# Optimization experiments

Hardware: AMD Instinct MI355X
Metric: run time of the kernel (lower is better)

Reference implementation:

```python
import jax, jax.numpy as jnp
import numpy as np

B, T, D, HD, HN, O = 32, 512, 512, 64, 16, 512
EPS = 1e-5


def setup_inputs() -> dict:
    key = jax.random.key(0)
    ks = jax.random.split(key, 12)
    s = lambda fan_in: 1.0 / np.sqrt(fan_in)
    inp = {
        "inputs": jax.random.normal(ks[0], (B, T, D), dtype=jnp.float32),
        "Wq": jax.random.uniform(ks[1], (HN, D, HD), jnp.float32, -s(D), s(D)),
        "bq": jnp.zeros((HN, HD), jnp.float32),
        "Wk": jax.random.uniform(ks[2], (HN, D, HD), jnp.float32, -s(D), s(D)),
        "bk": jnp.zeros((HN, HD), jnp.float32),
        "Wv": jax.random.uniform(ks[3], (HN, D, HD), jnp.float32, -s(D), s(D)),
        "bv": jnp.zeros((HN, HD), jnp.float32),
        "Wr": jax.random.uniform(ks[4], (D, O), jnp.float32, -s(D), s(D)),
        "br": jnp.zeros((O,), jnp.float32),
        "Wo": jax.random.uniform(ks[5], (HN * HD, O), jnp.float32, -s(HN * HD), s(HN * HD)),
        "bo": jnp.zeros((O,), jnp.float32),
        "ln1_w": jnp.ones((O,), jnp.float32),
        "ln1_b": jnp.zeros((O,), jnp.float32),
        "Wfc": jax.random.uniform(ks[6], (O, O), jnp.float32, -s(O), s(O)),
        "bfc": jnp.zeros((O,), jnp.float32),
        "ln2_w": jnp.ones((O,), jnp.float32),
        "ln2_b": jnp.zeros((O,), jnp.float32),
    }
    return inp


def _layernorm(x, w, b):
    mu = jnp.mean(x, axis=-1, keepdims=True)
    var = jnp.mean(jnp.square(x - mu), axis=-1, keepdims=True)
    return (x - mu) * jax.lax.rsqrt(var + EPS) * w + b


def reference(inputs, Wq, bq, Wk, bk, Wv, bv, Wr, br, Wo, bo,
              ln1_w, ln1_b, Wfc, bfc, ln2_w, ln2_b):
    # causal mask: multiply-then-subtract as in the original
    score_mask = jnp.tril(jnp.ones((T, T), jnp.float32))        # [T,T]
    padding_mask = (score_mask == 0).astype(jnp.float32) * 1e9  # [T,T]

    residual = inputs @ Wr + br                                  # [B,T,O]

    # batched per-head projections with nonstandard activations
    q = jax.nn.relu(jnp.einsum('btd,hdf->bhtf', inputs, Wq) + bq[None, :, None, :])
    k = jax.nn.relu(jnp.einsum('btd,hdf->bhtf', inputs, Wk) + bk[None, :, None, :])
    v = jnp.tanh(jnp.einsum('btd,hdf->bhtf', inputs, Wv) + bv[None, :, None, :])

    scores = jnp.einsum('bhtf,bhsf->bhts', q, k) / jnp.sqrt(jnp.float32(HD))
    scores = scores * score_mask - padding_mask                  # [B,H,T,T]
    weights = jax.nn.softmax(scores, axis=-1)
    heads = jnp.einsum('bhts,bhsf->bhtf', weights, v)            # [B,H,T,HD]

    # concat heads (head order preserved) + tanh output projection
    concat = heads.transpose(0, 2, 1, 3).reshape(B, T, HN * HD)
    out = jnp.tanh(concat @ Wo + bo)                             # [B,T,O]

    out = _layernorm(out + residual, ln1_w, ln1_b)
    fc = jax.nn.relu(out @ Wfc + bfc)
    out = _layernorm(fc + out, ln2_w, ln2_b)
    return out
```

## Files before the change

### kernel.cpp

```cpp
#include <hip/hip_runtime.h>
#include <hip/hip_bf16.h>

#define B_  32
#define T_  512
#define D_  512
#define HD_ 64
#define HN_ 16
#define O_  512
#define M_  (B_ * T_)
#define NQ_ (HN_ * HD_)

typedef __bf16 bf16;
typedef __attribute__((ext_vector_type(8))) __bf16 bf16x8;
typedef __attribute__((ext_vector_type(4))) __bf16 bf16x4;
typedef __attribute__((ext_vector_type(4))) float f32x4;

static __device__ __forceinline__ f32x4 mfma16(bf16x8 a, bf16x8 b, f32x4 c) {
    return __builtin_amdgcn_mfma_f32_16x16x32_bf16(a, b, c, 0, 0, 0);
}

static __device__ __forceinline__ void load_lds_16B(const bf16* g, bf16* l) {
    __builtin_amdgcn_global_load_lds(
        (const __attribute__((address_space(1))) unsigned int*)(unsigned long long)g,
        (__attribute__((address_space(3))) unsigned int*)(unsigned long long)l,
        16, 0, 0);
}

static __device__ __forceinline__ float fast_tanh(float x) {
    return 1.f - 2.f / (__expf(2.f * x) + 1.f);
}

static __device__ __forceinline__ int2 swz_block() {
    const int nx = gridDim.x;
    const int nwg = nx * gridDim.y;
    int l = blockIdx.y * nx + blockIdx.x;
    l = (l & 7) * (nwg >> 3) + (l >> 3);
    return make_int2(l % nx, l / nx);
}

__global__ __launch_bounds__(256) void prep_all_kernel(
    const float* __restrict__ inputs,
    const float* __restrict__ Wq, const float* __restrict__ Wk,
    const float* __restrict__ Wv, const float* __restrict__ Wr,
    const float* __restrict__ Wo, const float* __restrict__ Wfc,
    const float* __restrict__ bq, const float* __restrict__ bk,
    const float* __restrict__ bv, const float* __restrict__ br,
    bf16* __restrict__ xin, bf16* __restrict__ wall,
    bf16* __restrict__ wrt, bf16* __restrict__ wot, bf16* __restrict__ wfct,
    float* __restrict__ ball)
{
    __shared__ bf16 tl[64][72];
    const int tid = threadIdx.x;
    int id = blockIdx.x;

    if (id < 4096) {
        const size_t i = ((size_t)id * 256 + tid) * 8;
        f32x4 x0 = *(const f32x4*)(inputs + i);
        f32x4 x1 = *(const f32x4*)(inputs + i + 4);
        bf16x8 v;
        v[0] = (bf16)x0[0]; v[1] = (bf16)x0[1]; v[2] = (bf16)x0[2]; v[3] = (bf16)x0[3];
        v[4] = (bf16)x1[0]; v[5] = (bf16)x1[1]; v[6] = (bf16)x1[2]; v[7] = (bf16)x1[3];
        *(bf16x8*)(xin + i) = v;
        return;
    }
    if (id < 4480) {
        id -= 4096;
        const int kt = id & 7; id >>= 3;
        const int h = id & 15; id >>= 4;
        const float* src = (id == 0) ? Wq : (id == 1) ? Wk : Wv;
        bf16* dst = wall + (size_t)id * (1024 * 512);
        const int k0 = kt * 64;
#pragma unroll
        for (int i = 0; i < 4; i++) {
            const int e = i * 256 + tid;
            const int kk = e >> 4, f4 = (e & 15) * 4;
            const f32x4 v = *(const f32x4*)(src + ((size_t)h * 512 + k0 + kk) * 64 + f4);
#pragma unroll
            for (int j = 0; j < 4; j++) tl[f4 + j][kk] = (bf16)v[j];
        }
        __syncthreads();
#pragma unroll
        for (int i = 0; i < 2; i++) {
            const int e = i * 256 + tid;
            const int f = e >> 3, kc = (e & 7) * 8;
            *(bf16x8*)(dst + ((size_t)h * 64 + f) * 512 + k0 + kc) = *(const bf16x8*)&tl[f][kc];
        }
        return;
    }
    if (id < 4736) {
        id -= 4480;
        const float* src; bf16* dst; int K;
        if (id < 64)       { src = Wr;  dst = wrt;  K = 512;  }
        else if (id < 192) { src = Wo;  dst = wot;  K = 1024; id -= 64; }
        else               { src = Wfc; dst = wfct; K = 512;  id -= 192; }
        const int kt = id >> 3, nt = id & 7;
        const int k0 = kt * 64, n0 = nt * 64;
#pragma unroll
        for (int i = 0; i < 4; i++) {
            const int e = i * 256 + tid;
            const int kk = e >> 4, n4 = (e & 15) * 4;
            const f32x4 v = *(const f32x4*)(src + (size_t)(k0 + kk) * 512 + n0 + n4);
#pragma unroll
            for (int j = 0; j < 4; j++) tl[n4 + j][kk] = (bf16)v[j];
        }
        __syncthreads();
#pragma unroll
        for (int i = 0; i < 2; i++) {
            const int e = i * 256 + tid;
            const int nn = e >> 3, kc = (e & 7) * 8;
            *(bf16x8*)(dst + (size_t)(n0 + nn) * K + k0 + kc) = *(const bf16x8*)&tl[nn][kc];
        }
        return;
    }
    const int i = (id - 4736) * 256 + tid;
    float v = (i < 1024) ? bq[i]
            : (i < 2048) ? bk[i - 1024]
            : (i < 3072) ? bv[i - 2048] : br[i - 3072];
    ball[i] = v;
}

__global__ __launch_bounds__(512, 2) void gemm_qkvr256_kernel(
    const bf16* __restrict__ A, const bf16* __restrict__ Wall,
    const float* __restrict__ ball,
    bf16* __restrict__ qc, bf16* __restrict__ kb, bf16* __restrict__ vt,
    bf16* __restrict__ resb)
{
    __shared__ bf16 SL[65536];
    const int tid = threadIdx.x;
    const int lane = tid & 63;
    const int w = tid >> 6;
    const int wm = w >> 2, wn = w & 3;
    const int lr = lane & 15, lg = lane >> 4;
    const int K = 512;

    const int2 bc = swz_block();
    const int m0 = bc.y * 256, n0 = bc.x * 256;

    const int p = tid & 7;
    const int rr = tid >> 3;
    const int g = p ^ (rr & 7);
    const int arow0 = rr, arow1 = 128 + rr;
    const int brow0 = ((rr >> 5) << 6) | (rr & 31);
    const int brow1 = 128 + brow0;

    auto STAGE_H = [&](int t, int h) {
        const int slot = t & 1;
        const int k0 = t << 6;
        if ((h & 1) == 0) {
            bf16* Bb = SL + 32768 + slot * 16384;
            const int off = (h == 2) ? 32 : 0;
            const int r0_ = brow0 + off, r1_ = brow1 + off;
            load_lds_16B(Wall + (size_t)(n0 + r0_) * K + k0 + g * 8, Bb + r0_ * 64 + p * 8);
            load_lds_16B(Wall + (size_t)(n0 + r1_) * K + k0 + g * 8, Bb + r1_ * 64 + p * 8);
        } else {
            bf16* Ab = SL + slot * 16384;
            const int off = (h == 3) ? 64 : 0;
            const int r0_ = arow0 + off, r1_ = arow1 + off;
            load_lds_16B(A + (size_t)(m0 + r0_) * K + k0 + g * 8, Ab + r0_ * 64 + p * 8);
            load_lds_16B(A + (size_t)(m0 + r1_) * K + k0 + g * 8, Ab + r1_ * 64 + p * 8);
        }
    };

    const int x = lr & 7;
    auto LDA = [&](int t, int mi, int kc) -> bf16x8 {
        const int row = wm * 128 + mi * 16 + lr;
        const bf16* Ab = SL + (t & 1) * 16384;
        return *(const bf16x8*)&Ab[row * 64 + ((((kc << 2) | lg) ^ x) << 3)];
    };
    auto LDB = [&](int t, int nj, int kc) -> bf16x8 {
        const int row = wn * 64 + nj * 16 + lr;
        const bf16* Bb = SL + 32768 + (t & 1) * 16384;
        return *(const bf16x8*)&Bb[row * 64 + ((((kc << 2) | lg) ^ x) << 3)];
    };

    f32x4 acc[8][4];
    const f32x4 zero4 = {0.f, 0.f, 0.f, 0.f};
#pragma unroll
    for (int i = 0; i < 8; i++)
#pragma unroll
        for (int j = 0; j < 4; j++) acc[i][j] = zero4;

    bf16x8 b01[4], b23[4], af[8];

    STAGE_H(0, 0); STAGE_H(0, 1); STAGE_H(0, 2); STAGE_H(0, 3);

    for (int t = 0; t < 7; t++) {
        asm volatile("s_waitcnt vmcnt(4)\n\ts_barrier" ::: "memory");
#pragma unroll
        for (int nj = 0; nj < 2; nj++)
#pragma unroll
            for (int kc = 0; kc < 2; kc++) b01[nj * 2 + kc] = LDB(t, nj, kc);
#pragma unroll
        for (int mi = 0; mi < 4; mi++)
#pragma unroll
            for (int kc = 0; kc < 2; kc++) af[mi * 2 + kc] = LDA(t, mi, kc);
        STAGE_H(t + 1, 0);
        __builtin_amdgcn_s_setprio(1);
#pragma unroll
        for (int mi = 0; mi < 4; mi++)
#pragma unroll
            for (int nj = 0; nj < 2; nj++)
#pragma unroll
                for (int kc = 0; kc < 2; kc++)
                    acc[mi][nj] = mfma16(af[mi * 2 + kc], b01[nj * 2 + kc], acc[mi][nj]);
        __builtin_amdgcn_s_setprio(0);
        asm volatile("s_waitcnt vmcnt(4)\n\ts_barrier" ::: "memory");
#pragma unroll
        for (int nj = 0; nj < 2; nj++)
#pragma unroll
            for (int kc = 0; kc < 2; kc++) b23[nj * 2 + kc] = LDB(t, nj + 2, kc);
        STAGE_H(t + 1, 1);
        __builtin_amdgcn_s_setprio(1);
#pragma unroll
        for (int mi = 0; mi < 4; mi++)
#pragma unroll
            for (int nj = 0; nj < 2; nj++)
#pragma unroll
                for (int kc = 0; kc < 2; kc++)
                    acc[mi][nj + 2] = mfma16(af[mi * 2 + kc], b23[nj * 2 + kc], acc[mi][nj + 2]);
        __builtin_amdgcn_s_setprio(0);
        asm volatile("s_waitcnt vmcnt(4)\n\ts_barrier" ::: "memory");
#pragma unroll
        for (int mi = 0; mi < 4; mi++)
#pragma unroll
            for (int kc = 0; kc < 2; kc++) af[mi * 2 + kc] = LDA(t, mi + 4, kc);
        STAGE_H(t + 1, 2);
        __builtin_amdgcn_s_setprio(1);
#pragma unroll
        for (int mi = 0; mi < 4; mi++)
#pragma unroll
            for (int nj = 0; nj < 2; nj++)
#pragma unroll
                for (int kc = 0; kc < 2; kc++)
                    acc[mi + 4][nj] = mfma16(af[mi * 2 + kc], b01[nj * 2 + kc], acc[mi + 4][nj]);
        __builtin_amdgcn_s_setprio(0);
        STAGE_H(t + 1, 3);
        __builtin_amdgcn_s_setprio(1);
#pragma unroll
        for (int mi = 0; mi < 4; mi++)
#pragma unroll
            for (int nj = 0; nj < 2; nj++)
#pragma unroll
                for (int kc = 0; kc < 2; kc++)
                    acc[mi + 4][nj + 2] = mfma16(af[mi * 2 + kc], b23[nj * 2 + kc], acc[mi + 4][nj + 2]);
        __builtin_amdgcn_s_setprio(0);
    }

    {
        const int t = 7;
        asm volatile("s_waitcnt vmcnt(4)\n\ts_barrier" ::: "memory");
#pragma unroll
        for (int nj = 0; nj < 2; nj++)
#pragma unroll
            for (int kc = 0; kc < 2; kc++) b01[nj * 2 + kc] = LDB(t, nj, kc);
#pragma unroll
        for (int mi = 0; mi < 4; mi++)
#pragma unroll
            for (int kc = 0; kc < 2; kc++) af[mi * 2 + kc] = LDA(t, mi, kc);
        __builtin_amdgcn_s_setprio(1);
#pragma unroll
        for (int mi = 0; mi < 4; mi++)
#pragma unroll
            for (int nj = 0; nj < 2; nj++)
#pragma unroll
                for (int kc = 0; kc < 2; kc++)
                    acc[mi][nj] = mfma16(af[mi * 2 + kc], b01[nj * 2 + kc], acc[mi][nj]);
        __builtin_amdgcn_s_setprio(0);
        asm volatile("s_waitcnt vmcnt(2)\n\ts_barrier" ::: "memory");
#pragma unroll
        for (int nj = 0; nj < 2; nj++)
#pragma unroll
            for (int kc = 0; kc < 2; kc++) b23[nj * 2 + kc] = LDB(t, nj + 2, kc);
        __builtin_amdgcn_s_setprio(1);
#pragma unroll
        for (int mi = 0; mi < 4; mi++)
#pragma unroll
            for (int nj = 0; nj < 2; nj++)
#pragma unroll
                for (int kc = 0; kc < 2; kc++)
                    acc[mi][nj + 2] = mfma16(af[mi * 2 + kc], b23[nj * 2 + kc], acc[mi][nj + 2]);
        __builtin_amdgcn_s_setprio(0);
        asm volatile("s_waitcnt vmcnt(0)\n\ts_barrier" ::: "memory");
#pragma unroll
        for (int mi = 0; mi < 4; mi++)
#pragma unroll
            for (int kc = 0; kc < 2; kc++) af[mi * 2 + kc] = LDA(t, mi + 4, kc);
        __builtin_amdgcn_s_setprio(1);
#pragma unroll
        for (int mi = 0; mi < 4; mi++)
#pragma unroll
            for (int nj = 0; nj < 2; nj++)
#pragma unroll
                for (int kc = 0; kc < 2; kc++)
                    acc[mi + 4][nj] = mfma16(af[mi * 2 + kc], b01[nj * 2 + kc], acc[mi + 4][nj]);
#pragma unroll
        for (int mi = 0; mi < 4; mi++)
#pragma unroll
            for (int nj = 0; nj < 2; nj++)
#pragma unroll
                for (int kc = 0; kc < 2; kc++)
                    acc[mi + 4][nj + 2] = mfma16(af[mi * 2 + kc], b23[nj * 2 + kc], acc[mi + 4][nj + 2]);
        __builtin_amdgcn_s_setprio(0);
    }
    __syncthreads();

    const int region = n0 >> 10;
    if (region == 2) {
#pragma unroll
        for (int mi = 0; mi < 8; mi++) {
#pragma unroll
            for (int nj = 0; nj < 4; nj++) {
                const int n = n0 + wn * 64 + nj * 16 + lr;
                const float bn = ball[n];
                const int m = m0 + wm * 128 + mi * 16 + lg * 4;
                const int bb = m >> 9, tt = m & 511;
                const int nn = n - 2048, hh = nn >> 6, f = nn & 63;
                bf16x4 st;
#pragma unroll
                for (int r = 0; r < 4; r++) st[r] = (bf16)fast_tanh(acc[mi][nj][r] + bn);
                *(bf16x4*)(vt + (((size_t)(bb * 16 + hh) * 64 + f) << 9) + tt) = st;
            }
        }
    } else {
        bf16* dst; int pitch, nb; float scale = 1.f; bool rl = false;
        if (region == 0)      { dst = qc;   pitch = 1024; nb = n0;        scale = 0.125f; rl = true; }
        else if (region == 1) { dst = kb;   pitch = 1024; nb = n0 - 1024; rl = true; }
        else                  { dst = resb; pitch = 512;  nb = n0 - 3072; }
        float bn[4];
#pragma unroll
        for (int nj = 0; nj < 4; nj++) bn[nj] = ball[n0 + wn * 64 + nj * 16 + lr];
#pragma unroll
        for (int half = 0; half < 2; half++) {
            if (wm == half) {
#pragma unroll
                for (int mi = 0; mi < 8; mi++) {
#pragma unroll
                    for (int nj = 0; nj < 4; nj++) {
                        const int col = wn * 64 + nj * 16 + lr;
#pragma unroll
                        for (int r = 0; r < 4; r++) {
                            float v = acc[mi][nj][r] + bn[nj];
                            if (rl) v = fmaxf(v, 0.f);
                            SL[(mi * 16 + lg * 4 + r) * 264 + col] = (bf16)(v * scale);
                        }
                    }
                }
            }
            __syncthreads();
#pragma unroll
            for (int i = 0; i < 4; i++) {
                const int rr2 = i * 32 + (tid >> 4);
                const int cc = (tid & 15) * 16;
                bf16x8 v0 = *(const bf16x8*)&SL[rr2 * 264 + cc];
                bf16x8 v1 = *(const bf16x8*)&SL[rr2 * 264 + cc + 8];
                bf16* pdst = dst + (size_t)(m0 + half * 128 + rr2) * pitch + nb + cc;
                *(bf16x8*)pdst = v0;
                *(bf16x8*)(pdst + 8) = v1;
            }
            __syncthreads();
        }
    }
}

__device__ __forceinline__ void gemm_mainloop_p4(
    const bf16* __restrict__ A, const bf16* __restrict__ Wt,
    const int K, const int m0, const int n0, const int tid,
    bf16* SL, f32x4 (&acc)[4][4])
{
    const int lane = tid & 63;
    const int w = tid >> 6;
    const int wr = w >> 1, wc = w & 1;
    const int lr = lane & 15, lg = lane >> 4;
    const int nt = K >> 5;

    const int r0 = tid >> 2, s0 = tid & 3;
    const int g0 = s0 ^ ((r0 >> 1) & 3);
    const int r1 = r0 + 64;
    const int g1 = s0 ^ ((r1 >> 1) & 3);
    const bf16* aS0 = A + (size_t)(m0 + r0) * K + g0 * 8;
    const bf16* aS1 = A + (size_t)(m0 + r1) * K + g1 * 8;
    const bf16* bS0 = Wt + (size_t)(n0 + r0) * K + g0 * 8;
    const bf16* bS1 = Wt + (size_t)(n0 + r1) * K + g1 * 8;

    auto STAGE = [&](int t) {
        bf16* Ab = SL + (t & 3) * 4096;
        bf16* Bb = SL + 16384 + (t & 3) * 4096;
        const int k0 = t << 5;
        load_lds_16B(aS0 + k0, Ab + tid * 8);
        load_lds_16B(aS1 + k0, Ab + (tid + 256) * 8);
        load_lds_16B(bS0 + k0, Bb + tid * 8);
        load_lds_16B(bS1 + k0, Bb + (tid + 256) * 8);
    };

    STAGE(0); STAGE(1);
    asm volatile("s_waitcnt vmcnt(4)" ::: "memory");
    __builtin_amdgcn_s_barrier();

    for (int t = 0; t < nt; t++) {
        if (t + 2 < nt) {
            STAGE(t + 2);
            asm volatile("s_waitcnt vmcnt(4)" ::: "memory");
        } else {
            asm volatile("s_waitcnt vmcnt(0)" ::: "memory");
        }
        __builtin_amdgcn_s_barrier();

        const bf16* Ab = SL + (t & 3) * 4096;
        const bf16* Bb = SL + 16384 + (t & 3) * 4096;
        bf16x8 a[4], b[4];
#pragma unroll
        for (int mi = 0; mi < 4; mi++) {
            const int row = wr * 64 + mi * 16 + lr;
            a[mi] = *(const bf16x8*)&Ab[row * 32 + ((lg ^ ((row >> 1) & 3)) << 3)];
        }
#pragma unroll
        for (int nj = 0; nj < 4; nj++) {
            const int row = wc * 64 + nj * 16 + lr;
            b[nj] = *(const bf16x8*)&Bb[row * 32 + ((lg ^ ((row >> 1) & 3)) << 3)];
        }
        __builtin_amdgcn_s_setprio(1);
#pragma unroll
        for (int mi = 0; mi < 4; mi++)
#pragma unroll
            for (int nj = 0; nj < 4; nj++)
                acc[mi][nj] = mfma16(a[mi], b[nj], acc[mi][nj]);
        __builtin_amdgcn_s_setprio(0);
    }
    __builtin_amdgcn_s_barrier();
}

template <int ACT>
__global__ __launch_bounds__(256) void gemm_std_kernel(
    const bf16* __restrict__ A, const bf16* __restrict__ Wt,
    const float* __restrict__ bias, bf16* __restrict__ C, const int K)
{
    __shared__ bf16 SL[32768];
    const int tid = threadIdx.x;
    const int2 bc = swz_block();
    const int m0 = bc.y * 128, n0 = bc.x * 128;
    f32x4 acc[4][4];
    const f32x4 zero4 = {0.f, 0.f, 0.f, 0.f};
#pragma unroll
    for (int i = 0; i < 4; i++)
#pragma unroll
        for (int j = 0; j < 4; j++) acc[i][j] = zero4;

    gemm_mainloop_p4(A, Wt, K, m0, n0, tid, SL, acc);

    const int lane = tid & 63, w = tid >> 6;
    const int wr = w >> 1, wc = w & 1, lr = lane & 15, lg = lane >> 4;
#pragma unroll
    for (int mi = 0; mi < 4; mi++) {
#pragma unroll
        for (int nj = 0; nj < 4; nj++) {
            const float bn = bias[n0 + wc * 64 + nj * 16 + lr];
            const int rbase = wr * 64 + mi * 16 + lg * 4;
            const int cidx = wc * 64 + nj * 16 + lr;
#pragma unroll
            for (int r = 0; r < 4; r++) {
                float v = acc[mi][nj][r] + bn;
                if constexpr (ACT == 1) v = fmaxf(v, 0.f);
                else if constexpr (ACT == 2) v = fast_tanh(v);
                SL[(rbase + r) * 136 + cidx] = (bf16)v;
            }
        }
    }
    __syncthreads();
#pragma unroll
    for (int pass = 0; pass < 4; pass++) {
        const int rr = pass * 32 + (tid >> 3);
        const int cc = (tid & 7) * 16;
        bf16x8 v0 = *(const bf16x8*)&SL[rr * 136 + cc];
        bf16x8 v1 = *(const bf16x8*)&SL[rr * 136 + cc + 8];
        *(bf16x8*)(C + (size_t)(m0 + rr) * 512 + n0 + cc) = v0;
        *(bf16x8*)(C + (size_t)(m0 + rr) * 512 + n0 + cc + 8) = v1;
    }
}

static __device__ __forceinline__ int sigma_k(int t) {
    return (t & 32) | ((t & 4) << 2) | ((t & 24) >> 1) | (t & 3);
}

__global__ __launch_bounds__(256) void mfma_attn_kernel(
    const bf16* __restrict__ Kb, const bf16* __restrict__ Vt, bf16* __restrict__ QC)
{
    __shared__ bf16 Ks[2][64][72];
    __shared__ bf16 Vts[2][64][72];

    int l = blockIdx.x;
    l = (l & 7) * 256 + (l >> 3);
    const int qb = l & 3;
    const int h = (l >> 2) & 15;
    const int b = l >> 6;
    const int tid = threadIdx.x;
    const int lane = tid & 63;
    const int w = tid >> 6;
    const int lr = lane & 15, lg = lane >> 4;

    const int qrow0 = qb * 128 + w * 32;
    const size_t qbase = ((size_t)b * T_ + qrow0) * NQ_ + h * 64;
    const int bh = b * HN_ + h;

    bf16x8 qf[2][2];
#pragma unroll
    for (int mi = 0; mi < 2; mi++)
#pragma unroll
        for (int kc = 0; kc < 2; kc++)
            qf[mi][kc] = *(const bf16x8*)(QC + qbase + (size_t)(mi * 16 + lr) * NQ_ + kc * 32 + lg * 8);

    const f32x4 zero4 = {0.f, 0.f, 0.f, 0.f};
    f32x4 o[2][4];
    float m_st[2] = {-1e30f, -1e30f}, l_st[2] = {0.f, 0.f};
#pragma unroll
    for (int mi = 0; mi < 2; mi++)
#pragma unroll
        for (int dj = 0; dj < 4; dj++) o[mi][dj] = zero4;

    const int nsb = 2 * qb + 2;

    bf16x8 kreg[2], vreg[2];
    auto LOADR = [&](int sb) {
#pragma unroll
        for (int i = 0; i < 2; i++) {
            const int ci = i * 256 + tid, row = ci >> 3, cc = ci & 7;
            kreg[i] = *(const bf16x8*)(Kb + ((size_t)b * T_ + sb * 64 + row) * NQ_ + h * 64 + cc * 8);
            vreg[i] = *(const bf16x8*)(Vt + ((size_t)bh * 64 + row) * T_ + sb * 64 + cc * 8);
        }
    };
    auto WRITE = [&](int buf) {
#pragma unroll
        for (int i = 0; i < 2; i++) {
            const int ci = i * 256 + tid, row = ci >> 3, cc = ci & 7;
            *(bf16x8*)&Ks[buf][sigma_k(row)][cc * 8] = kreg[i];
            *(bf16x8*)&Vts[buf][row][cc * 8] = vreg[i];
        }
    };

    LOADR(0); WRITE(0); __syncthreads();
    int cur = 0;

    for (int sb = 0; sb < nsb; sb++) {
        const bool pf = (sb + 1 < nsb);
        if (pf) LOADR(sb + 1);

        if (sb * 64 <= qrow0 + 31) {
            f32x4 sc[2][4];
#pragma unroll
            for (int mi = 0; mi < 2; mi++)
#pragma unroll
                for (int nj = 0; nj < 4; nj++) sc[mi][nj] = zero4;
            __builtin_amdgcn_s_setprio(1);
#pragma unroll
            for (int kc = 0; kc < 2; kc++) {
                bf16x8 kf[4];
#pragma unroll
                for (int nj = 0; nj < 4; nj++)
                    kf[nj] = *(const bf16x8*)&Ks[cur][nj * 16 + lr][kc * 32 + lg * 8];
#pragma unroll
                for (int mi = 0; mi < 2; mi++)
#pragma unroll
                    for (int nj = 0; nj < 4; nj++)
                        sc[mi][nj] = mfma16(kf[nj], qf[mi][kc], sc[mi][nj]);
            }
            __builtin_amdgcn_s_setprio(0);
            const bool needmask = (sb * 64 + 63 > qrow0);
            float tm[2];
#pragma unroll
            for (int mi = 0; mi < 2; mi++) {
                const int qg = qrow0 + mi * 16 + lr;
                float mx = -1e30f;
#pragma unroll
                for (int nj = 0; nj < 4; nj++) {
                    const int kvb = sb * 64 + ((nj >> 1) << 5) + ((nj & 1) << 2) + lg * 8;
#pragma unroll
                    for (int r = 0; r < 4; r++) {
                        float s = sc[mi][nj][r];
                        if (needmask && (kvb + r > qg)) s = -1e30f;
                        sc[mi][nj][r] = s;
                        mx = fmaxf(mx, s);
                    }
                }
                mx = fmaxf(mx, __shfl_xor(mx, 16));
                mx = fmaxf(mx, __shfl_xor(mx, 32));
                tm[mi] = mx;
            }
            const bool defer = (tm[0] <= m_st[0] + 8.f) && (tm[1] <= m_st[1] + 8.f);
            if (!__all(defer)) {
#pragma unroll
                for (int mi = 0; mi < 2; mi++) {
                    const float mn = fmaxf(m_st[mi], tm[mi]);
                    const float sf = __expf(m_st[mi] - mn);
                    m_st[mi] = mn;
                    l_st[mi] *= sf;
#pragma unroll
                    for (int dj = 0; dj < 4; dj++)
#pragma unroll
                        for (int r = 0; r < 4; r++) o[mi][dj][r] *= sf;
                }
            }
            bf16x4 pk[2][4];
#pragma unroll
            for (int mi = 0; mi < 2; mi++) {
                float ts = 0.f;
#pragma unroll
                for (int nj = 0; nj < 4; nj++)
#pragma unroll
                    for (int r = 0; r < 4; r++) {
                        const float p2 = __expf(sc[mi][nj][r] - m_st[mi]);
                        ts += p2;
                        pk[mi][nj][r] = (bf16)p2;
                    }
                ts += __shfl_xor(ts, 16);
                ts += __shfl_xor(ts, 32);
                l_st[mi] += ts;
            }
            __builtin_amdgcn_s_setprio(1);
#pragma unroll
            for (int kc = 0; kc < 2; kc++) {
                bf16x8 vf[4], pf2[2];
#pragma unroll
                for (int mi = 0; mi < 2; mi++) {
                    bf16x8 t;
#pragma unroll
                    for (int r = 0; r < 4; r++) { t[r] = pk[mi][2 * kc][r]; t[r + 4] = pk[mi][2 * kc + 1][r]; }
                    pf2[mi] = t;
                }
#pragma unroll
                for (int dj = 0; dj < 4; dj++)
                    vf[dj] = *(const bf16x8*)&Vts[cur][dj * 16 + lr][kc * 32 + lg * 8];
#pragma unroll
                for (int mi = 0; mi < 2; mi++)
#pragma unroll
                    for (int dj = 0; dj < 4; dj++)
                        o[mi][dj] = mfma16(vf[dj], pf2[mi], o[mi][dj]);
            }
            __builtin_amdgcn_s_setprio(0);
        }

        if (pf) WRITE(cur ^ 1);
        __syncthreads();
        cur ^= 1;
    }

#pragma unroll
    for (int mi = 0; mi < 2; mi++) {
        const float inv = 1.f / l_st[mi];
        const size_t rowoff = qbase + (size_t)(mi * 16 + lr) * NQ_;
#pragma unroll
        for (int dj = 0; dj < 4; dj++) {
            bf16x4 st;
#pragma unroll
            for (int r = 0; r < 4; r++) st[r] = (bf16)(o[mi][dj][r] * inv);
            *(bf16x4*)(QC + rowoff + dj * 16 + lg * 4) = st;
        }
    }
}

template <bool F32OUT>
__global__ __launch_bounds__(256) void ln_kernel(
    const bf16* __restrict__ xa, const bf16* __restrict__ xb,
    const float* __restrict__ w, const float* __restrict__ bias,
    void* __restrict__ outv)
{
    const int row = blockIdx.x * 4 + (threadIdx.x >> 6);
    const int ln = threadIdx.x & 63;
    const size_t base = (size_t)row * 512 + ln * 8;
    const bf16x8 va = *(const bf16x8*)(xa + base);
    const bf16x8 vb = *(const bf16x8*)(xb + base);
    float x[8];
    float s = 0.f;
#pragma unroll
    for (int i = 0; i < 8; i++) { x[i] = (float)va[i] + (float)vb[i]; s += x[i]; }
#pragma unroll
    for (int off = 32; off >= 1; off >>= 1) s += __shfl_xor(s, off);
    const float mean = s * (1.f / 512.f);
    float ss = 0.f;
#pragma unroll
    for (int i = 0; i < 8; i++) { x[i] -= mean; ss += x[i] * x[i]; }
#pragma unroll
    for (int off = 32; off >= 1; off >>= 1) ss += __shfl_xor(ss, off);
    const float inv = rsqrtf(ss * (1.f / 512.f) + 1e-5f);
    const f32x4 w0 = *(const f32x4*)(w + ln * 8);
    const f32x4 w1 = *(const f32x4*)(w + ln * 8 + 4);
    const f32x4 b0 = *(const f32x4*)(bias + ln * 8);
    const f32x4 b1 = *(const f32x4*)(bias + ln * 8 + 4);
    if constexpr (F32OUT) {
        f32x4 y0, y1;
#pragma unroll
        for (int i = 0; i < 4; i++) {
            y0[i] = x[i] * inv * w0[i] + b0[i];
            y1[i] = x[4 + i] * inv * w1[i] + b1[i];
        }
        *(f32x4*)((float*)outv + base) = y0;
        *(f32x4*)((float*)outv + base + 4) = y1;
    } else {
        bf16x8 y;
#pragma unroll
        for (int i = 0; i < 4; i++) {
            y[i] = (bf16)(x[i] * inv * w0[i] + b0[i]);
            y[4 + i] = (bf16)(x[4 + i] * inv * w1[i] + b1[i]);
        }
        *(bf16x8*)((bf16*)outv + base) = y;
    }
}

extern "C" void kernel_launch(void* const* d_in, const int* in_sizes, int n_in,
                              void* d_out, int out_size, void* d_ws, size_t ws_size,
                              hipStream_t stream)
{
    const float* inputs = (const float*)d_in[0];
    const float* Wq = (const float*)d_in[1];
    const float* bq = (const float*)d_in[2];
    const float* Wk = (const float*)d_in[3];
    const float* bk = (const float*)d_in[4];
    const float* Wv = (const float*)d_in[5];
    const float* bv = (const float*)d_in[6];
    const float* Wr = (const float*)d_in[7];
    const float* br = (const float*)d_in[8];
    const float* Wo = (const float*)d_in[9];
    const float* bo = (const float*)d_in[10];
    const float* ln1w = (const float*)d_in[11];
    const float* ln1b = (const float*)d_in[12];
    const float* Wfc = (const float*)d_in[13];
    const float* bfc = (const float*)d_in[14];
    const float* ln2w = (const float*)d_in[15];
    const float* ln2b = (const float*)d_in[16];
    float* out = (float*)d_out;

    const size_t MB = 1024ull * 1024ull;
    char* ws = (char*)d_ws;
    bf16* qc   = (bf16*)(ws);
    bf16* kb   = (bf16*)(ws + 32 * MB);
    bf16* vt   = (bf16*)(ws + 64 * MB);
    bf16* xin  = (bf16*)(ws + 96 * MB);
    bf16* wall = (bf16*)(ws + 112 * MB);
    bf16* wot  = (bf16*)(ws + 112 * MB + 3670016);
    bf16* wfct = (bf16*)(ws + 112 * MB + 3670016 + 1048576);
    float* ball = (float*)(ws + 112 * MB + 3670016 + 1048576 + 524288);
    bf16* wrt  = wall + (size_t)3072 * 512;
    bf16* resb = (bf16*)d_out;
    bf16* att  = kb;
    bf16* ln1  = kb + (size_t)8 * MB;
    bf16* fcb  = vt;

    const dim3 blk(256);

    prep_all_kernel<<<dim3(4750), blk, 0, stream>>>(
        inputs, Wq, Wk, Wv, Wr, Wo, Wfc, bq, bk, bv, br,
        xin, wall, wrt, wot, wfct, ball);

    gemm_qkvr256_kernel<<<dim3(14, 64), dim3(512), 0, stream>>>(
        xin, wall, ball, qc, kb, vt, resb);
    mfma_attn_kernel<<<dim3(B_ * HN_ * 4), blk, 0, stream>>>(kb, vt, qc);
    gemm_std_kernel<2><<<dim3(4, 128), blk, 0, stream>>>(qc, wot, bo, att, 1024);
    ln_kernel<false><<<dim3(4096), blk, 0, stream>>>(att, resb, ln1w, ln1b, ln1);
    gemm_std_kernel<1><<<dim3(4, 128), blk, 0, stream>>>(ln1, wfct, bfc, fcb, 512);
    ln_kernel<true ><<<dim3(4096), blk, 0, stream>>>(fcb, ln1, ln2w, ln2b, out);
}
```

Baseline: 244.7 us.

## Fuse output-projection and FC GEMMs with residual add and LayerNorm

Replaces the two 128x128-tile GEMM kernels and the two separate LayerNorm kernels with a single templated kernel. Each block computes a full 64x512 row tile, so residual add, bias, activation and LayerNorm can all happen in the epilogue. Row statistics are reduced across lanes and waves through shared memory. This removes the intermediate GEMM-output round trips through global memory and two kernel launches. In exchange it uses about 147KB of LDS per block, allowing only one 4-wave block per CU with a 256-block grid. Every block also streams the whole weight matrix, and variance is computed as E[x^2]-mean^2, which is less numerically robust.

```diff
diff --git a/kernel.cpp b/kernel.cpp
--- a/kernel.cpp
+++ b/kernel.cpp
@@ -362,118 +362,188 @@
     }
 }
 
-__device__ __forceinline__ void gemm_mainloop_p4(
+template <int ACT, bool F32OUT>
+__global__ __launch_bounds__(256) void gemm_ln_kernel(
     const bf16* __restrict__ A, const bf16* __restrict__ Wt,
-    const int K, const int m0, const int n0, const int tid,
-    bf16* SL, f32x4 (&acc)[4][4])
+    const float* __restrict__ bias, const bf16* __restrict__ partner,
+    const float* __restrict__ lnw, const float* __restrict__ lnb,
+    void* __restrict__ outv, const int K)
 {
+    __shared__ bf16 SL[73728];
+    __shared__ float parts[2][4][64];
+    const int tid = threadIdx.x;
     const int lane = tid & 63;
     const int w = tid >> 6;
-    const int wr = w >> 1, wc = w & 1;
     const int lr = lane & 15, lg = lane >> 4;
+    const int m0 = blockIdx.x * 64;
     const int nt = K >> 5;
 
-    const int r0 = tid >> 2, s0 = tid & 3;
-    const int g0 = s0 ^ ((r0 >> 1) & 3);
-    const int r1 = r0 + 64;
-    const int g1 = s0 ^ ((r1 >> 1) & 3);
-    const bf16* aS0 = A + (size_t)(m0 + r0) * K + g0 * 8;
-    const bf16* aS1 = A + (size_t)(m0 + r1) * K + g1 * 8;
-    const bf16* bS0 = Wt + (size_t)(n0 + r0) * K + g0 * 8;
-    const bf16* bS1 = Wt + (size_t)(n0 + r1) * K + g1 * 8;
+    const int srow = tid >> 2, s0 = tid & 3;
+    const int g = s0 ^ ((srow >> 1) & 3);
+    const bf16* aP = A + (size_t)(m0 + srow) * K + g * 8;
+    const bf16* bP = Wt + (size_t)srow * K + g * 8;
 
     auto STAGE = [&](int t) {
-        bf16* Ab = SL + (t & 3) * 4096;
-        bf16* Bb = SL + 16384 + (t & 3) * 4096;
+        bf16* Ab = SL + (t & 3) * 2048;
+        bf16* Bb = SL + 8192 + (t & 3) * 16384;
         const int k0 = t << 5;
-        load_lds_16B(aS0 + k0, Ab + tid * 8);
-        load_lds_16B(aS1 + k0, Ab + (tid + 256) * 8);
-        load_lds_16B(bS0 + k0, Bb + tid * 8);
-        load_lds_16B(bS1 + k0, Bb + (tid + 256) * 8);
+        load_lds_16B(aP + k0, Ab + tid * 8);
+#pragma unroll
+        for (int j = 0; j < 8; j++)
+            load_lds_16B(bP + k0 + (size_t)(j * 64) * K, Bb + (tid + j * 256) * 8);
     };
 
+    f32x4 acc[4][8];
+    const f32x4 zero4 = {0.f, 0.f, 0.f, 0.f};
+#pragma unroll
+    for (int i = 0; i < 4; i++)
+#pragma unroll
+        for (int j = 0; j < 8; j++) acc[i][j] = zero4;
+
     STAGE(0); STAGE(1);
-    asm volatile("s_waitcnt vmcnt(4)" ::: "memory");
+    asm volatile("s_waitcnt vmcnt(9)" ::: "memory");
     __builtin_amdgcn_s_barrier();
 
     for (int t = 0; t < nt; t++) {
         if (t + 2 < nt) {
             STAGE(t + 2);
-            asm volatile("s_waitcnt vmcnt(4)" ::: "memory");
+            asm volatile("s_waitcnt vmcnt(9)" ::: "memory");
         } else {
             asm volatile("s_waitcnt vmcnt(0)" ::: "memory");
         }
         __builtin_amdgcn_s_barrier();
 
-        const bf16* Ab = SL + (t & 3) * 4096;
-        const bf16* Bb = SL + 16384 + (t & 3) * 4096;
-        bf16x8 a[4], b[4];
+        const bf16* Ab = SL + (t & 3) * 2048;
+        const bf16* Bb = SL + 8192 + (t & 3) * 16384;
+        bf16x8 a[4], b[8];
 #pragma unroll
         for (int mi = 0; mi < 4; mi++) {
-            const int row = wr * 64 + mi * 16 + lr;
+            const int row = mi * 16 + lr;
             a[mi] = *(const bf16x8*)&Ab[row * 32 + ((lg ^ ((row >> 1) & 3)) << 3)];
         }
 #pragma unroll
-        for (int nj = 0; nj < 4; nj++) {
-            const int row = wc * 64 + nj * 16 + lr;
+        for (int nj = 0; nj < 8; nj++) {
+            const int row = w * 128 + nj * 16 + lr;
             b[nj] = *(const bf16x8*)&Bb[row * 32 + ((lg ^ ((row >> 1) & 3)) << 3)];
         }
         __builtin_amdgcn_s_setprio(1);
 #pragma unroll
         for (int mi = 0; mi < 4; mi++)
 #pragma unroll
-            for (int nj = 0; nj < 4; nj++)
+            for (int nj = 0; nj < 8; nj++)
                 acc[mi][nj] = mfma16(a[mi], b[nj], acc[mi][nj]);
         __builtin_amdgcn_s_setprio(0);
     }
-    __builtin_amdgcn_s_barrier();
-}
-
-template <int ACT>
-__global__ __launch_bounds__(256) void gemm_std_kernel(
-    const bf16* __restrict__ A, const bf16* __restrict__ Wt,
-    const float* __restrict__ bias, bf16* __restrict__ C, const int K)
-{
-    __shared__ bf16 SL[32768];
-    const int tid = threadIdx.x;
-    const int2 bc = swz_block();
-    const int m0 = bc.y * 128, n0 = bc.x * 128;
-    f32x4 acc[4][4];
-    const f32x4 zero4 = {0.f, 0.f, 0.f, 0.f};
-#pragma unroll
-    for (int i = 0; i < 4; i++)
-#pragma unroll
-        for (int j = 0; j < 4; j++) acc[i][j] = zero4;
-
-    gemm_mainloop_p4(A, Wt, K, m0, n0, tid, SL, acc);
-
-    const int lane = tid & 63, w = tid >> 6;
-    const int wr = w >> 1, wc = w & 1, lr = lane & 15, lg = lane >> 4;
-#pragma unroll
-    for (int mi = 0; mi < 4; mi++) {
-#pragma unroll
-        for (int nj = 0; nj < 4; nj++) {
-            const float bn = bias[n0 + wc * 64 + nj * 16 + lr];
-            const int rbase = wr * 64 + mi * 16 + lg * 4;
-            const int cidx = wc * 64 + nj * 16 + lr;
+    __syncthreads();
+
+    bf16* SLp = SL;
+#pragma unroll
+    for (int jj = 0; jj < 16; jj++) {
+        const int e = jj * 256 + tid;
+        const int row = e >> 6, col = (e & 63) * 8;
+        *(bf16x8*)&SLp[row * 520 + col] =
+            *(const bf16x8*)(partner + (size_t)(m0 + row) * 512 + col);
+    }
+    __syncthreads();
+
+    float bn[8], lw[8], lb[8];
+#pragma unroll
+    for (int nj = 0; nj < 8; nj++) {
+        const int col = w * 128 + nj * 16 + lr;
+        bn[nj] = bias[col]; lw[nj] = lnw[col]; lb[nj] = lnb[col];
+    }
+
+    float rs[16], rq[16];
+#pragma unroll
+    for (int i = 0; i < 16; i++) { rs[i] = 0.f; rq[i] = 0.f; }
+#pragma unroll
+    for (int mi = 0; mi < 4; mi++)
+#pragma unroll
+        for (int r = 0; r < 4; r++) {
+            const int row = mi * 16 + lg * 4 + r;
+            float ps = 0.f, pq = 0.f;
+#pragma unroll
+            for (int nj = 0; nj < 8; nj++) {
+                float x = acc[mi][nj][r] + bn[nj];
+                if constexpr (ACT == 1) x = fmaxf(x, 0.f);
+                else if constexpr (ACT == 2) x = fast_tanh(x);
+                x += (float)SLp[row * 520 + w * 128 + nj * 16 + lr];
+                acc[mi][nj][r] = x;
+                ps += x; pq += x * x;
+            }
+            rs[mi * 4 + r] = ps; rq[mi * 4 + r] = pq;
+        }
+#pragma unroll
+    for (int i = 0; i < 16; i++) {
+#pragma unroll
+        for (int off = 1; off <= 8; off <<= 1) {
+            rs[i] += __shfl_xor(rs[i], off);
+            rq[i] += __shfl_xor(rq[i], off);
+        }
+    }
+    if (lr == 0) {
+#pragma unroll
+        for (int mi = 0; mi < 4; mi++)
 #pragma unroll
             for (int r = 0; r < 4; r++) {
-                float v = acc[mi][nj][r] + bn;
-                if constexpr (ACT == 1) v = fmaxf(v, 0.f);
-                else if constexpr (ACT == 2) v = fast_tanh(v);
-                SL[(rbase + r) * 136 + cidx] = (bf16)v;
-            }
-        }
+                const int row = mi * 16 + lg * 4 + r;
+                parts[0][w][row] = rs[mi * 4 + r];
+                parts[1][w][row] = rq[mi * 4 + r];
+            }
     }
     __syncthreads();
-#pragma unroll
-    for (int pass = 0; pass < 4; pass++) {
-        const int rr = pass * 32 + (tid >> 3);
-        const int cc = (tid & 7) * 16;
-        bf16x8 v0 = *(const bf16x8*)&SL[rr * 136 + cc];
-        bf16x8 v1 = *(const bf16x8*)&SL[rr * 136 + cc + 8];
-        *(bf16x8*)(C + (size_t)(m0 + rr) * 512 + n0 + cc) = v0;
-        *(bf16x8*)(C + (size_t)(m0 + rr) * 512 + n0 + cc + 8) = v1;
+
+    float mean_[16], inv_[16];
+#pragma unroll
+    for (int mi = 0; mi < 4; mi++)
+#pragma unroll
+        for (int r = 0; r < 4; r++) {
+            const int row = mi * 16 + lg * 4 + r;
+            const float S = parts[0][0][row] + parts[0][1][row] + parts[0][2][row] + parts[0][3][row];
+            const float Q = parts[1][0][row] + parts[1][1][row] + parts[1][2][row] + parts[1][3][row];
+            const float m = S * (1.f / 512.f);
+            mean_[mi * 4 + r] = m;
+            inv_[mi * 4 + r] = rsqrtf(Q * (1.f / 512.f) - m * m + 1e-5f);
+        }
+
+    if constexpr (F32OUT) {
+        float* outp = (float*)outv;
+#pragma unroll
+        for (int mi = 0; mi < 4; mi++)
+#pragma unroll
+            for (int r = 0; r < 4; r++) {
+                const int row = mi * 16 + lg * 4 + r;
+                const float m = mean_[mi * 4 + r], iv = inv_[mi * 4 + r];
+#pragma unroll
+                for (int nj = 0; nj < 8; nj++) {
+                    const int col = w * 128 + nj * 16 + lr;
+                    outp[(size_t)(m0 + row) * 512 + col] =
+                        (acc[mi][nj][r] - m) * iv * lw[nj] + lb[nj];
+                }
+            }
+    } else {
+        bf16* SLy = SL + 36864;
+#pragma unroll
+        for (int mi = 0; mi < 4; mi++)
+#pragma unroll
+            for (int r = 0; r < 4; r++) {
+                const int row = mi * 16 + lg * 4 + r;
+                const float m = mean_[mi * 4 + r], iv = inv_[mi * 4 + r];
+#pragma unroll
+                for (int nj = 0; nj < 8; nj++) {
+                    const int col = w * 128 + nj * 16 + lr;
+                    SLy[row * 520 + col] = (bf16)((acc[mi][nj][r] - m) * iv * lw[nj] + lb[nj]);
+                }
+            }
+        __syncthreads();
+        bf16* outp = (bf16*)outv;
+#pragma unroll
+        for (int jj = 0; jj < 16; jj++) {
+            const int e = jj * 256 + tid;
+            const int row = e >> 6, col = (e & 63) * 8;
+            *(bf16x8*)(outp + (size_t)(m0 + row) * 512 + col) =
+                *(const bf16x8*)&SLy[row * 520 + col];
+        }
     }
 }
 
@@ -653,54 +723,6 @@
             for (int r = 0; r < 4; r++) st[r] = (bf16)(o[mi][dj][r] * inv);
             *(bf16x4*)(QC + rowoff + dj * 16 + lg * 4) = st;
         }
-    }
-}
-
-template <bool F32OUT>
-__global__ __launch_bounds__(256) void ln_kernel(
-    const bf16* __restrict__ xa, const bf16* __restrict__ xb,
-    const float* __restrict__ w, const float* __restrict__ bias,
-    void* __restrict__ outv)
-{
-    const int row = blockIdx.x * 4 + (threadIdx.x >> 6);
-    const int ln = threadIdx.x & 63;
-    const size_t base = (size_t)row * 512 + ln * 8;
-    const bf16x8 va = *(const bf16x8*)(xa + base);
-    const bf16x8 vb = *(const bf16x8*)(xb + base);
-    float x[8];
-    float s = 0.f;
-#pragma unroll
-    for (int i = 0; i < 8; i++) { x[i] = (float)va[i] + (float)vb[i]; s += x[i]; }
-#pragma unroll
-    for (int off = 32; off >= 1; off >>= 1) s += __shfl_xor(s, off);
-    const float mean = s * (1.f / 512.f);
-    float ss = 0.f;
-#pragma unroll
-    for (int i = 0; i < 8; i++) { x[i] -= mean; ss += x[i] * x[i]; }
-#pragma unroll
-    for (int off = 32; off >= 1; off >>= 1) ss += __shfl_xor(ss, off);
-    const float inv = rsqrtf(ss * (1.f / 512.f) + 1e-5f);
-    const f32x4 w0 = *(const f32x4*)(w + ln * 8);
-    const f32x4 w1 = *(const f32x4*)(w + ln * 8 + 4);
-    const f32x4 b0 = *(const f32x4*)(bias + ln * 8);
-    const f32x4 b1 = *(const f32x4*)(bias + ln * 8 + 4);
-    if constexpr (F32OUT) {
-        f32x4 y0, y1;
-#pragma unroll
-        for (int i = 0; i < 4; i++) {
-            y0[i] = x[i] * inv * w0[i] + b0[i];
-            y1[i] = x[4 + i] * inv * w1[i] + b1[i];
-        }
-        *(f32x4*)((float*)outv + base) = y0;
-        *(f32x4*)((float*)outv + base + 4) = y1;
-    } else {
-        bf16x8 y;
-#pragma unroll
-        for (int i = 0; i < 4; i++) {
-            y[i] = (bf16)(x[i] * inv * w0[i] + b0[i]);
-            y[4 + i] = (bf16)(x[4 + i] * inv * w1[i] + b1[i]);
-        }
-        *(bf16x8*)((bf16*)outv + base) = y;
     }
 }
 
@@ -737,23 +759,20 @@
     bf16* wot  = (bf16*)(ws + 112 * MB + 3670016);
     bf16* wfct = (bf16*)(ws + 112 * MB + 3670016 + 1048576);
     float* ball = (float*)(ws + 112 * MB + 3670016 + 1048576 + 524288);
-    bf16* wrt  = wall + (size_t)3072 * 512;
     bf16* resb = (bf16*)d_out;
-    bf16* att  = kb;
     bf16* ln1  = kb + (size_t)8 * MB;
-    bf16* fcb  = vt;
 
     const dim3 blk(256);
 
     prep_all_kernel<<<dim3(4750), blk, 0, stream>>>(
         inputs, Wq, Wk, Wv, Wr, Wo, Wfc, bq, bk, bv, br,
-        xin, wall, wrt, wot, wfct, ball);
+        xin, wall, wall + (size_t)3072 * 512, wot, wfct, ball);
 
     gemm_qkvr256_kernel<<<dim3(14, 64), dim3(512), 0, stream>>>(
         xin, wall, ball, qc, kb, vt, resb);
     mfma_attn_kernel<<<dim3(B_ * HN_ * 4), blk, 0, stream>>>(kb, vt, qc);
-    gemm_std_kernel<2><<<dim3(4, 128), blk, 0, stream>>>(qc, wot, bo, att, 1024);
-    ln_kernel<false><<<dim3(4096), blk, 0, stream>>>(att, resb, ln1w, ln1b, ln1);
-    gemm_std_kernel<1><<<dim3(4, 128), blk, 0, stream>>>(ln1, wfct, bfc, fcb, 512);
-    ln_kernel<true ><<<dim3(4096), blk, 0, stream>>>(fcb, ln1, ln2w, ln2b, out);
-}
+    gemm_ln_kernel<2, false><<<dim3(256), blk, 0, stream>>>(
+        qc, wot, bo, resb, ln1w, ln1b, ln1, 1024);
+    gemm_ln_kernel<1, true><<<dim3(256), blk, 0, stream>>>(
+        ln1, wfct, bfc, ln1, ln2w, ln2b, out, 512);
+}
```

Result: no change. 246.6 us (+0.8%).
